# Performance work log

Hardware: AMD Instinct MI355X
Metric: run time of the kernel (lower is better)

## Reference

```python
import jax, jax.numpy as jnp
import numpy as np

N = 100000   # nodes
D = 256      # in_dim == out_dim
R = 4        # num_rel
T = 150000   # triangles per relation
H = 2        # nheads (num_rel >= 2)
DH = D // H
EPS = 1e-5


def _layernorm(x, g, b):
    m = jnp.mean(x, axis=-1, keepdims=True)
    v = jnp.mean((x - m) ** 2, axis=-1, keepdims=True)
    return (x - m) * jax.lax.rsqrt(v + EPS) * g + b


def setup_inputs() -> dict:
    key = jax.random.key(0)
    ks = jax.random.split(key, 24)
    s = 1.0 / np.sqrt(D)
    f32 = jnp.float32
    inp = {}
    inp["x"] = jax.random.normal(ks[0], (N, D), f32)
    inp["triangles"] = jax.random.randint(ks[1], (R, 3, T), 0, N)
    inp["edge_index"] = jax.random.randint(ks[2], (R, 2, 8), 0, N)
    inp["node_W"] = jax.random.normal(ks[3], (R, D, D), f32) * s
    inp["tri_W"] = jax.random.normal(ks[4], (R, D, D), f32) * s
    inp["res_W"] = jax.random.normal(ks[5], (D, D), f32) * s
    inp["gate_W"] = jax.random.normal(ks[6], (D, 2 * D), f32) * (1.0 / np.sqrt(2 * D))
    inp["gate_b"] = jnp.zeros((D,), f32)
    inp["in_W"] = jax.random.normal(ks[7], (3 * D, D), f32) * s
    inp["in_b"] = jnp.zeros((3 * D,), f32)
    inp["out_W"] = jax.random.normal(ks[8], (D, D), f32) * s
    inp["out_b"] = jnp.zeros((D,), f32)
    inp["ln1_g"] = jnp.ones((D,), f32)
    inp["ln1_b"] = jnp.zeros((D,), f32)
    inp["lin1_W"] = jax.random.normal(ks[9], (2 * D, D), f32) * s
    inp["lin1_b"] = jnp.zeros((2 * D,), f32)
    inp["lin2_W"] = jax.random.normal(ks[10], (D, 2 * D), f32) * (1.0 / np.sqrt(2 * D))
    inp["lin2_b"] = jnp.zeros((D,), f32)
    inp["ln2_g"] = jnp.ones((D,), f32)
    inp["ln2_b"] = jnp.zeros((D,), f32)
    return inp


def reference(x, triangles, edge_index, node_W, tri_W, res_W, gate_W, gate_b,
              in_W, in_b, out_W, out_b, ln1_g, ln1_b,
              lin1_W, lin1_b, lin2_W, lin2_b, ln2_g, ln2_b):
    del edge_index  # unused by the original forward
    x_res = x @ res_W.T  # [N, D]
    hs = []
    for r in range(R):  # small fixed relation count
        tri = triangles[r]                                 # [3, T]
        tri_feat = (x[tri] @ node_W[r].T).mean(axis=0)     # [T, D]
        tri_msg = tri_feat @ tri_W[r].T                    # [T, D]
        idx = tri.T.reshape(-1)                            # [3T], triangle-major
        rep = jnp.repeat(tri_msg, 3, axis=0)               # [3T, D]
        ssum = jax.ops.segment_sum(rep, idx, num_segments=N)
        cnt = jax.ops.segment_sum(jnp.ones((3 * T,), x.dtype), idx, num_segments=N)
        node_msg = ssum / jnp.maximum(cnt, 1.0)[:, None]   # scatter_mean
        u = jax.nn.elu(node_msg)                           # dropout = identity (eval)
        a = jax.nn.sigmoid(jnp.concatenate([x, u], axis=1) @ gate_W.T + gate_b)
        hs.append(jnp.tanh(u) * a + x_res * (1.0 - a))
    src = jnp.stack(hs, axis=0)                            # [R, N, D] (seq, batch, d)

    # single post-norm TransformerEncoderLayer over the relation axis
    qkv = src @ in_W.T + in_b                              # [R, N, 3D]
    q, k, v = jnp.split(qkv, 3, axis=-1)
    q = q.reshape(R, N, H, DH)
    k = k.reshape(R, N, H, DH)
    v = v.reshape(R, N, H, DH)
    scores = jnp.einsum('qnhd,knhd->nhqk', q, k) / np.sqrt(DH)
    attn = jax.nn.softmax(scores, axis=-1)
    o = jnp.einsum('nhqk,knhd->qnhd', attn, v).reshape(R, N, D)
    o = o @ out_W.T + out_b
    x1 = _layernorm(src + o, ln1_g, ln1_b)
    ff = jax.nn.gelu(x1 @ lin1_W.T + lin1_b, approximate=False) @ lin2_W.T + lin2_b
    x2 = _layernorm(x1 + ff, ln2_g, ln2_b)
    return x2.mean(axis=0)                                 # [N, D]
```

## Files before the change

### kernel.cpp

```cpp
#include <hip/hip_runtime.h>


#define NNODES 100000
#define NPAD   100096
#define DIM    256
#define NREL   4
#define NTRI   150000
#define NPART  8
#define PSIZE  (NPAD / NPART)

typedef unsigned short ushortT;
typedef __attribute__((ext_vector_type(8)))  short   short8;
typedef __attribute__((ext_vector_type(4)))  float   floatx4;
typedef __attribute__((ext_vector_type(4)))  unsigned short ushort4v;

__device__ __forceinline__ float bf2f(ushortT u) {
    union { unsigned int i; float f; } c; c.i = ((unsigned int)u) << 16; return c.f;
}
__device__ __forceinline__ ushortT f2bf(float f) {
    union { float f; unsigned int i; } c; c.f = f;
    unsigned int x = c.i;
    x += 0x7fffu + ((x >> 16) & 1u);
    return (ushortT)(x >> 16);
}
__device__ __forceinline__ float erf_as(float x) {
    float ax = fabsf(x);
    float k  = 1.0f / (1.0f + 0.3275911f * ax);
    float p  = k * (0.254829592f + k * (-0.284496736f + k * (1.421413741f +
               k * (-1.453152027f + k * 1.061405429f))));
    float r  = 1.0f - p * __expf(-ax * ax);
    return copysignf(r, x);
}


__global__ void cvt_f32_bf16(const float* __restrict__ in, ushortT* __restrict__ out, int n4) {
    int i = blockIdx.x * blockDim.x + threadIdx.x;
    int stride = gridDim.x * blockDim.x;
    for (; i < n4; i += stride) {
        float4 v = ((const float4*)in)[i];
        ushort4v o; o.x = f2bf(v.x); o.y = f2bf(v.y); o.z = f2bf(v.z); o.w = f2bf(v.w);
        ((ushort4v*)out)[i] = o;
    }
}

__global__ void wcomb_kernel(const float* __restrict__ nodeW, const float* __restrict__ triW,
                             ushortT* __restrict__ wcomb) {
    int idx = blockIdx.x * 256 + threadIdx.x;
    int r = idx >> 16, o = (idx >> 8) & 255, k = idx & 255;
    const float* tw = triW  + ((size_t)r << 16) + o * 256;
    const float* nw = nodeW + ((size_t)r << 16) + k;
    float s = 0.f;
    #pragma unroll 8
    for (int j = 0; j < 256; ++j) s += tw[j] * nw[(size_t)j * 256];
    wcomb[idx] = f2bf(s);
}

__global__ void pack_xg(const float* __restrict__ resW, const float* __restrict__ gateW,
                        ushortT* __restrict__ o) {
    int idx = blockIdx.x * 256 + threadIdx.x;
    int r = idx >> 8, k = idx & 255;
    float v = (r < 256) ? resW[r * 256 + k] : gateW[(size_t)(r - 256) * 512 + k];
    o[idx] = f2bf(v);
}

__global__ void pack_wvo(const float* __restrict__ outW, const float* __restrict__ inW,
                         ushortT* __restrict__ o) {
    int idx = blockIdx.x * 256 + threadIdx.x;
    int r = idx >> 8, k = idx & 255;
    int orow = r & 255, d0 = (r >> 8) * 128;
    float s = 0.f;
    #pragma unroll 8
    for (int j = 0; j < 128; ++j)
        s += outW[orow * 256 + d0 + j] * inW[(size_t)(512 + d0 + j) * 256 + k];
    o[idx] = f2bf(s);
}

__global__ void calc_bvo(const float* __restrict__ outW, const float* __restrict__ in_b,
                         float* __restrict__ bvo) {
    int c = blockIdx.x * 256 + threadIdx.x;
    int orow = c & 255, d0 = (c >> 8) * 128;
    float s = 0.f;
    #pragma unroll 8
    for (int j = 0; j < 128; ++j) s += outW[orow * 256 + d0 + j] * in_b[512 + d0 + j];
    bvo[c] = s;
}


__global__ void k_count8(const int* __restrict__ tri, int* __restrict__ cnt4, int n3) {
    int r = blockIdx.y;
    int part = blockIdx.x & 7;
    int i = (blockIdx.x >> 3) * 256 + threadIdx.x;
    if (i >= n3) return;
    int node = tri[(size_t)r * n3 + i];
    if (node / PSIZE != part) return;
    atomicAdd(&cnt4[r * NPAD + node], 1);
}

__global__ void k_scan1(const int* __restrict__ cnt4, int* __restrict__ ptr4,
                        int* __restrict__ bsum4, int n) {
    int r = blockIdx.y;
    const int* cnt = cnt4 + r * NPAD;
    int* ptr = ptr4 + r * NPAD;
    int* bsum = bsum4 + r * 512;
    __shared__ int s[256];
    int i = blockIdx.x * 256 + threadIdx.x;
    int v = (i < n) ? cnt[i] : 0;
    s[threadIdx.x] = v; __syncthreads();
    for (int off = 1; off < 256; off <<= 1) {
        int t = (threadIdx.x >= off) ? s[threadIdx.x - off] : 0;
        __syncthreads();
        s[threadIdx.x] += t;
        __syncthreads();
    }
    if (i < n) ptr[i] = s[threadIdx.x] - v;
    if (threadIdx.x == 255) bsum[blockIdx.x] = s[255];
}

__global__ void k_scan2(const int* __restrict__ bsum4, int* __restrict__ bpre4, int nb) {
    int r = blockIdx.x;
    const int* bsum = bsum4 + r * 512;
    int* bpre = bpre4 + r * 512;
    int lane = threadIdx.x & 63;
    int run = 0;
    for (int c = 0; c < nb; c += 64) {
        int idx = c + lane;
        int v = (idx < nb) ? bsum[idx] : 0;
        int incl = v;
        #pragma unroll
        for (int off = 1; off < 64; off <<= 1) {
            int t = __shfl_up(incl, off, 64);
            if (lane >= off) incl += t;
        }
        if (idx < nb) bpre[idx] = run + incl - v;
        run += __shfl(incl, 63, 64);
    }
}

__global__ void k_scan3(const int* __restrict__ bpre4, int* __restrict__ ptr4,
                        int* __restrict__ cur4, int n) {
    int r = blockIdx.y;
    int i = blockIdx.x * 256 + threadIdx.x;
    if (i < n) {
        int p = ptr4[r * NPAD + i] + bpre4[r * 512 + blockIdx.x];
        ptr4[r * NPAD + i] = p; cur4[r * NPAD + i] = p;
    }
}

__global__ void k_fill8(const int* __restrict__ tri, int* __restrict__ cur4,
                        int* __restrict__ adj4, int n3, int T) {
    int r = blockIdx.y;
    int part = blockIdx.x & 7;
    int i = (blockIdx.x >> 3) * 256 + threadIdx.x;
    if (i >= n3) return;
    int node = tri[(size_t)r * n3 + i];
    if (node / PSIZE != part) return;
    int t = i; if (t >= 2 * T) t -= 2 * T; else if (t >= T) t -= T;
    int pos = atomicAdd(&cur4[r * NPAD + node], 1);
    adj4[(size_t)r * n3 + pos] = t;
}

__global__ __launch_bounds__(256)
void k_meanx(const int* __restrict__ tri, const ushortT* __restrict__ xb,
             ushortT* __restrict__ mx, int T) {
    int t = blockIdx.x * 4 + (threadIdx.x >> 6);
    if (t >= T) return;
    int lane = threadIdx.x & 63;
    int a = tri[t], b = tri[T + t], c = tri[2 * T + t];
    ushort4v va = *(const ushort4v*)(xb + (size_t)a * DIM + lane * 4);
    ushort4v vb = *(const ushort4v*)(xb + (size_t)b * DIM + lane * 4);
    ushort4v vc = *(const ushort4v*)(xb + (size_t)c * DIM + lane * 4);
    ushort4v o;
    o.x = f2bf((bf2f(va.x) + bf2f(vb.x) + bf2f(vc.x)) * (1.0f / 3.0f));
    o.y = f2bf((bf2f(va.y) + bf2f(vb.y) + bf2f(vc.y)) * (1.0f / 3.0f));
    o.z = f2bf((bf2f(va.z) + bf2f(vb.z) + bf2f(vc.z)) * (1.0f / 3.0f));
    o.w = f2bf((bf2f(va.w) + bf2f(vb.w) + bf2f(vc.w)) * (1.0f / 3.0f));
    *(ushort4v*)(mx + (size_t)t * DIM + lane * 4) = o;
}

__global__ __launch_bounds__(256)
void k_gather(const int* __restrict__ ptr, const int* __restrict__ cnt,
              const int* __restrict__ adj, const ushortT* __restrict__ mx,
              ushortT* __restrict__ accb, int n) {
    int node = blockIdx.x * 4 + (threadIdx.x >> 6);
    if (node >= n) return;
    int lane = threadIdx.x & 63;
    int st = ptr[node], c = cnt[node];
    float a0 = 0.f, a1 = 0.f, a2 = 0.f, a3 = 0.f;
    for (int j = 0; j < c; ++j) {
        int t = adj[st + j];
        ushort4v v = *(const ushort4v*)(mx + (size_t)t * DIM + lane * 4);
        a0 += bf2f(v.x); a1 += bf2f(v.y); a2 += bf2f(v.z); a3 += bf2f(v.w);
    }
    float inv = 1.0f / fmaxf((float)c, 1.0f);
    ushort4v o; o.x = f2bf(a0 * inv); o.y = f2bf(a1 * inv);
    o.z = f2bf(a2 * inv); o.w = f2bf(a3 * inv);
    *(ushort4v*)(accb + (size_t)node * DIM + lane * 4) = o;
}


#define BK 32
#define PADW 133

__device__ __forceinline__ void async_cp16(char* lds, const char* glb) {
    __builtin_amdgcn_global_load_lds((const __attribute__((address_space(1))) unsigned int*)glb,
                                     (__attribute__((address_space(3))) unsigned int*)lds,
                                     16, 0, 0);
}

enum { M_BF16 = 0, M_ELU = 1, M_GATE = 2, M_QKV = 3, M_RES = 4, M_GELU = 5 };

template <int MODE>
__global__ __launch_bounds__(256)
void gemm_bt(const ushortT* __restrict__ A, int lda, size_t aStrZ,
             const ushortT* __restrict__ W, int ldw, size_t wStrZ,
             int M, int K,
             ushortT* __restrict__ outB, int ldo, size_t oStrZ,
             const float* __restrict__ bias,
             const ushortT* __restrict__ aux1,
             const ushortT* __restrict__ aux2,
             int auxLd,
             const ushortT* __restrict__ resB,
             size_t resStrZ) {
    const size_t zi = blockIdx.z;
    A += zi * aStrZ; W += zi * wStrZ;
    if (outB) outB += zi * oStrZ;
    if (resB) resB += zi * resStrZ;

    __shared__ __align__(16) char smem[49152];
    const int tid  = threadIdx.x;
    const int wave = tid >> 6, lane = tid & 63;
    const int m0 = blockIdx.y * 128;
    const int n0 = blockIdx.x * 128;
    const int wm = (wave >> 1) * 64, wn = (wave & 1) * 64;

    floatx4 acc[4][4];
    #pragma unroll
    for (int i = 0; i < 4; ++i)
        #pragma unroll
        for (int j = 0; j < 4; ++j) acc[i][j] = (floatx4){0.f, 0.f, 0.f, 0.f};

    const int r4  = tid >> 2;
    const int b16 = (tid & 3) * 16;
    const char* Ab = (const char*)A + ((size_t)(m0 + r4) * lda) * 2 + b16;
    const char* Wb = (const char*)W + ((size_t)(n0 + r4) * ldw) * 2 + b16;

    const int kq = (lane >> 4) * 8;
    const int ra = wm + (lane & 15);
    const int rb = wn + (lane & 15);

    auto stage = [&](int buf, int k0) {
        char* Asl = smem + buf * 8192 + wave * 1024;
        char* Bsl = smem + 24576 + buf * 8192 + wave * 1024;
        async_cp16(Asl,        Ab + k0 * 2);
        async_cp16(Asl + 4096, Ab + k0 * 2 + (size_t)64 * lda * 2);
        async_cp16(Bsl,        Wb + k0 * 2);
        async_cp16(Bsl + 4096, Wb + k0 * 2 + (size_t)64 * ldw * 2);
    };
    auto compute = [&](int buf) {
        const ushortT* Abuf = (const ushortT*)(smem + buf * 8192);
        const ushortT* Bbuf = (const ushortT*)(smem + 24576 + buf * 8192);
        short8 af[4], bfr[4];
        #pragma unroll
        for (int i = 0; i < 4; ++i) {
            af[i]  = *(const short8*)(Abuf + (ra + i * 16) * BK + kq);
            bfr[i] = *(const short8*)(Bbuf + (rb + i * 16) * BK + kq);
        }
        #pragma unroll
        for (int mi = 0; mi < 4; ++mi)
            #pragma unroll
            for (int ni = 0; ni < 4; ++ni)
                acc[mi][ni] = __builtin_amdgcn_mfma_f32_16x16x32_bf16(af[mi], bfr[ni], acc[mi][ni], 0, 0, 0);
    };

    const int NIT = K / BK;
    stage(0, 0);
    stage(1, BK);
    asm volatile("s_waitcnt vmcnt(4)" ::: "memory");
    __builtin_amdgcn_s_barrier();

    int bufc = 0, bufs = 2;
    for (int it = 0; it < NIT; ++it) {
        if (it + 2 < NIT) stage(bufs, (it + 2) * BK);
        compute(bufc);
        if (it + 1 < NIT) {
            if (it + 2 < NIT) asm volatile("s_waitcnt vmcnt(4)" ::: "memory");
            else              asm volatile("s_waitcnt vmcnt(0)" ::: "memory");
            __builtin_amdgcn_s_barrier();
        }
        bufc = (bufc == 2) ? 0 : bufc + 1;
        bufs = (bufs == 2) ? 0 : bufs + 1;
    }

    __syncthreads();
    float* Ct = (float*)smem;
    const int cl = lane & 15, rw = (lane >> 4) * 4;
    const int lr = tid >> 2;
    const int cb = (tid & 3) * 32;
    #pragma unroll
    for (int p = 0; p < 2; ++p) {
        if (wm == p * 64) {
            #pragma unroll
            for (int mi = 0; mi < 4; ++mi)
                #pragma unroll
                for (int ni = 0; ni < 4; ++ni)
                    #pragma unroll
                    for (int e = 0; e < 4; ++e)
                        Ct[(mi * 16 + rw + e) * PADW + (wn + ni * 16 + cl)] = acc[mi][ni][e];
        }
        __syncthreads();
        const int m = m0 + p * 64 + lr;
        if (m < M) {
            #pragma unroll
            for (int k8 = 0; k8 < 4; ++k8) {
                const int c0  = cb + k8 * 8;
                const int col = n0 + c0;
                float v[8];
                #pragma unroll
                for (int j = 0; j < 8; ++j) v[j] = Ct[lr * PADW + c0 + j];
                short8 ov;
                if (MODE == M_BF16) {
                    #pragma unroll
                    for (int j = 0; j < 8; ++j) ov[j] = (short)f2bf(v[j]);
                } else if (MODE == M_ELU) {
                    #pragma unroll
                    for (int j = 0; j < 8; ++j) {
                        float c = v[j] > 0.f ? v[j] : (__expf(v[j]) - 1.0f);
                        ov[j] = (short)f2bf(c);
                    }
                } else if (MODE == M_GATE) {
                    short8 gv = *(const short8*)(aux1 + (size_t)m * auxLd + col);
                    short8 xv = *(const short8*)(aux2 + (size_t)m * auxLd + col);
                    short8 uv = *(const short8*)(A + (size_t)m * lda + col);
                    #pragma unroll
                    for (int j = 0; j < 8; ++j) {
                        float g  = bf2f((ushortT)gv[j]);
                        float xr = bf2f((ushortT)xv[j]);
                        float u  = bf2f((ushortT)uv[j]);
                        float a  = 1.0f / (1.0f + __expf(-(v[j] + g + bias[col + j])));
                        float th = 1.0f - 2.0f / (__expf(2.0f * u) + 1.0f);
                        ov[j] = (short)f2bf(th * a + xr * (1.0f - a));
                    }
                } else if (MODE == M_QKV) {
                    #pragma unroll
                    for (int j = 0; j < 8; ++j) ov[j] = (short)f2bf(v[j] + bias[col + j]);
                } else if (MODE == M_RES) {
                    short8 rv = *(const short8*)(resB + (size_t)m * 256 + col);
                    #pragma unroll
                    for (int j = 0; j < 8; ++j)
                        ov[j] = (short)f2bf(v[j] + bias[col + j] + bf2f((ushortT)rv[j]));
                } else if (MODE == M_GELU) {
                    #pragma unroll
                    for (int j = 0; j < 8; ++j) {
                        float t = v[j] + bias[col + j];
                        ov[j] = (short)f2bf(0.5f * t * (1.0f + erf_as(t * 0.70710678118f)));
                    }
                }
                *(short8*)(&outB[(size_t)m * ldo + col]) = ov;
            }
        }
        if (p == 0) __syncthreads();
    }
}

__global__ __launch_bounds__(256)
void attn_score(const ushortT* __restrict__ qk, size_t rstride,
                float* __restrict__ Aw, int nvalid) {
    int n = blockIdx.x * 4 + (threadIdx.x >> 6);
    if (n >= nvalid) return;
    int lane = threadIdx.x & 63;
    int head = lane >> 5, hl = lane & 31;
    int d = head * 128 + hl * 4;
    float q[NREL][4], k[NREL][4];
    #pragma unroll
    for (int r = 0; r < NREL; ++r) {
        const ushortT* base = qk + r * rstride + (size_t)n * 512;
        ushort4v qv = *(const ushort4v*)(base + d);
        ushort4v kv = *(const ushort4v*)(base + 256 + d);
        q[r][0] = bf2f(qv.x); q[r][1] = bf2f(qv.y); q[r][2] = bf2f(qv.z); q[r][3] = bf2f(qv.w);
        k[r][0] = bf2f(kv.x); k[r][1] = bf2f(kv.y); k[r][2] = bf2f(kv.z); k[r][3] = bf2f(kv.w);
    }
    float s[NREL][NREL];
    #pragma unroll
    for (int qr = 0; qr < NREL; ++qr)
        #pragma unroll
        for (int kr = 0; kr < NREL; ++kr) {
            float p = q[qr][0] * k[kr][0] + q[qr][1] * k[kr][1] +
                      q[qr][2] * k[kr][2] + q[qr][3] * k[kr][3];
            #pragma unroll
            for (int off = 1; off < 32; off <<= 1) p += __shfl_xor(p, off, 32);
            s[qr][kr] = p * 0.08838834764831845f;
        }
    if (hl < 16) {
        int qr = hl >> 2, kr = hl & 3;
        float mx = fmaxf(fmaxf(s[qr][0], s[qr][1]), fmaxf(s[qr][2], s[qr][3]));
        float e0 = __expf(s[qr][0] - mx), e1 = __expf(s[qr][1] - mx);
        float e2 = __expf(s[qr][2] - mx), e3 = __expf(s[qr][3] - mx);
        float e  = __expf(s[qr][kr] - mx);
        Aw[((size_t)n * 2 + head) * 16 + qr * 4 + kr] = e / (e0 + e1 + e2 + e3);
    }
}

__global__ __launch_bounds__(256)
void attn_combine_ln1(const ushortT* __restrict__ vo4, size_t rstride,
                      const ushortT* __restrict__ h4, size_t hstride,
                      const float* __restrict__ Aw,
                      const float* __restrict__ ob,
                      const float* __restrict__ g, const float* __restrict__ b,
                      ushortT* __restrict__ x1, size_t x1str, int nvalid) {
    int n = blockIdx.x * 4 + (threadIdx.x >> 6);
    if (n >= nvalid) return;
    int lane = threadIdx.x & 63;
    int d4 = lane * 4;
    const float* ap = Aw + (size_t)n * 32;
    float a0[NREL][NREL], a1[NREL][NREL];
    #pragma unroll
    for (int qr = 0; qr < NREL; ++qr)
        #pragma unroll
        for (int kr = 0; kr < NREL; ++kr) {
            a0[qr][kr] = ap[qr * 4 + kr];
            a1[qr][kr] = ap[16 + qr * 4 + kr];
        }
    float vl[NREL][4], vh[NREL][4];
    #pragma unroll
    for (int kr = 0; kr < NREL; ++kr) {
        const ushortT* base = vo4 + kr * rstride + (size_t)n * 512;
        ushort4v lo = *(const ushort4v*)(base + d4);
        ushort4v hi = *(const ushort4v*)(base + 256 + d4);
        vl[kr][0] = bf2f(lo.x); vl[kr][1] = bf2f(lo.y); vl[kr][2] = bf2f(lo.z); vl[kr][3] = bf2f(lo.w);
        vh[kr][0] = bf2f(hi.x); vh[kr][1] = bf2f(hi.y); vh[kr][2] = bf2f(hi.z); vh[kr][3] = bf2f(hi.w);
    }
    float bb0 = ob[d4], bb1 = ob[d4 + 1], bb2 = ob[d4 + 2], bb3 = ob[d4 + 3];
    float g0 = g[d4], g1 = g[d4 + 1], g2 = g[d4 + 2], g3 = g[d4 + 3];
    float e0 = b[d4], e1 = b[d4 + 1], e2 = b[d4 + 2], e3 = b[d4 + 3];
    #pragma unroll
    for (int qr = 0; qr < NREL; ++qr) {
        ushort4v hv = *(const ushort4v*)(h4 + qr * hstride + (size_t)n * 256 + d4);
        float z0 = bf2f(hv.x) + bb0, z1 = bf2f(hv.y) + bb1;
        float z2 = bf2f(hv.z) + bb2, z3 = bf2f(hv.w) + bb3;
        #pragma unroll
        for (int kr = 0; kr < NREL; ++kr) {
            float c0 = a0[qr][kr], c1 = a1[qr][kr];
            z0 += c0 * vl[kr][0] + c1 * vh[kr][0];
            z1 += c0 * vl[kr][1] + c1 * vh[kr][1];
            z2 += c0 * vl[kr][2] + c1 * vh[kr][2];
            z3 += c0 * vl[kr][3] + c1 * vh[kr][3];
        }
        float s = z0 + z1 + z2 + z3;
        #pragma unroll
        for (int off = 1; off < 64; off <<= 1) s += __shfl_xor(s, off, 64);
        float mean = s * (1.0f / 256.0f);
        float dx = z0 - mean, dy = z1 - mean, dz = z2 - mean, dw = z3 - mean;
        float qs = dx * dx + dy * dy + dz * dz + dw * dw;
        #pragma unroll
        for (int off = 1; off < 64; off <<= 1) qs += __shfl_xor(qs, off, 64);
        float rstd = rsqrtf(qs * (1.0f / 256.0f) + 1e-5f);
        ushort4v o;
        o.x = f2bf(dx * rstd * g0 + e0); o.y = f2bf(dy * rstd * g1 + e1);
        o.z = f2bf(dz * rstd * g2 + e2); o.w = f2bf(dw * rstd * g3 + e3);
        *(ushort4v*)(x1 + qr * x1str + (size_t)n * 256 + d4) = o;
    }
}

__global__ __launch_bounds__(256)
void ln2_out(const ushortT* __restrict__ zb, size_t zStrZ,
             const float* __restrict__ g, const float* __restrict__ b,
             float* __restrict__ outc, int n) {
    int row = blockIdx.x * 4 + (threadIdx.x >> 6);
    if (row >= n) return;
    int lane = threadIdx.x & 63, c0 = lane * 4;
    float g0 = g[c0], g1 = g[c0 + 1], g2 = g[c0 + 2], g3 = g[c0 + 3];
    float b0 = b[c0], b1 = b[c0 + 1], b2 = b[c0 + 2], b3 = b[c0 + 3];
    float o0 = 0.f, o1 = 0.f, o2 = 0.f, o3 = 0.f;
    #pragma unroll
    for (int r = 0; r < NREL; ++r) {
        ushort4v v = *(const ushort4v*)(zb + r * zStrZ + (size_t)row * 256 + c0);
        float vx = bf2f(v.x), vy = bf2f(v.y), vz = bf2f(v.z), vw = bf2f(v.w);
        float s = vx + vy + vz + vw;
        #pragma unroll
        for (int off = 1; off < 64; off <<= 1) s += __shfl_xor(s, off, 64);
        float mean = s * (1.0f / 256.0f);
        float dx = vx - mean, dy = vy - mean, dz = vz - mean, dw = vw - mean;
        float qs = dx * dx + dy * dy + dz * dz + dw * dw;
        #pragma unroll
        for (int off = 1; off < 64; off <<= 1) qs += __shfl_xor(qs, off, 64);
        float rstd = rsqrtf(qs * (1.0f / 256.0f) + 1e-5f);
        o0 += 0.25f * (dx * rstd * g0 + b0);
        o1 += 0.25f * (dy * rstd * g1 + b1);
        o2 += 0.25f * (dz * rstd * g2 + b2);
        o3 += 0.25f * (dw * rstd * g3 + b3);
    }
    float4 o; o.x = o0; o.y = o1; o.z = o2; o.w = o3;
    *(float4*)(outc + (size_t)row * 256 + c0) = o;
}


extern "C" void kernel_launch(void* const* d_in, const int* in_sizes, int n_in,
                              void* d_out, int out_size, void* d_ws, size_t ws_size,
                              hipStream_t stream) {
    const float* x      = (const float*)d_in[0];
    const int*   tri    = (const int*)d_in[1];
    const float* nodeW  = (const float*)d_in[3];
    const float* triW   = (const float*)d_in[4];
    const float* resW   = (const float*)d_in[5];
    const float* gateW  = (const float*)d_in[6];
    const float* gate_b = (const float*)d_in[7];
    const float* inW    = (const float*)d_in[8];
    const float* in_b   = (const float*)d_in[9];
    const float* outW   = (const float*)d_in[10];
    const float* out_b  = (const float*)d_in[11];
    const float* ln1g   = (const float*)d_in[12];
    const float* ln1b   = (const float*)d_in[13];
    const float* lin1W  = (const float*)d_in[14];
    const float* lin1b  = (const float*)d_in[15];
    const float* lin2W  = (const float*)d_in[16];
    const float* lin2b  = (const float*)d_in[17];
    const float* ln2g   = (const float*)d_in[18];
    const float* ln2b   = (const float*)d_in[19];
    float* out = (float*)d_out;

    char* ws = (char*)d_ws;
    size_t off = 0;
    auto alloc = [&](size_t bytes) -> char* {
        char* p = ws + off; off += (bytes + 255) & ~(size_t)255; return p;
    };
    ushortT* accAll  = (ushortT*)alloc((size_t)NREL * NPAD * 256 * 2);
    ushortT* xall_b  = (ushortT*)alloc((size_t)NPAD * 256 * 2);
    ushortT* wcomb   = (ushortT*)alloc((size_t)NREL * 65536 * 2);
    ushortT* xgW_b   = (ushortT*)alloc((size_t)131072 * 2);
    ushortT* gateW_b = (ushortT*)alloc((size_t)131072 * 2);
    ushortT* inW_b   = (ushortT*)alloc((size_t)131072 * 2);
    ushortT* wvo_b   = (ushortT*)alloc((size_t)131072 * 2);
    ushortT* lin1_bf = (ushortT*)alloc((size_t)131072 * 2);
    ushortT* lin2_bf = (ushortT*)alloc((size_t)131072 * 2);
    float*   bvo     = (float*)  alloc((size_t)512 * 4);
    size_t persist = off;
    size_t scratch = (ws_size > persist) ? (ws_size - persist) : 0;
    char* S = ws + persist;

    int*     cnt4  = (int*)(S);
    int*     ptr4  = cnt4 + 4 * NPAD;
    int*     cur4  = ptr4 + 4 * NPAD;
    int*     bsum4 = cur4 + 4 * NPAD;
    int*     bpre4 = bsum4 + 4 * 512;
    int*     adj4  = bpre4 + 4 * 512;
    size_t csrBytes = ((char*)(adj4 + (size_t)4 * 3 * NTRI) - S + 255) & ~(size_t)255;
    const size_t mxBytes = (size_t)NTRI * 256 * 2;
    if (scratch < csrBytes + mxBytes + 65536) return;
    ushortT* mxbf = (ushortT*)(S + csrBytes);

    const size_t ROWB = 9344;
    int TT = (NNODES + 127) / 128;
    int tpcMax = (int)(scratch / (ROWB * 128));
    if (tpcMax < 1) return;
    if (tpcMax > TT) tpcMax = TT;
    const int nchunks = (TT + tpcMax - 1) / tpcMax;
    const int tpc = (TT + nchunks - 1) / nchunks;
    const size_t NcPad = (size_t)tpc * 128;

    ushortT* xg   = (ushortT*)(S);
    ushortT* ubf4 = (ushortT*)(S + 1024 * NcPad);
    ushortT* h4   = (ushortT*)(S + 3072 * NcPad);
    ushortT* qk4  = (ushortT*)(S + 5120 * NcPad);
    ushortT* vo4  = qk4;
    ushortT* x1   = (ushortT*)(S);
    ushortT* ffg  = (ushortT*)(S + 2048 * NcPad);
    ushortT* zbb  = (ushortT*)(S + 6144 * NcPad);
    float*   Aw   = (float*)  (S + 9216 * NcPad);

    cvt_f32_bf16<<<2048, 256, 0, stream>>>(x, xall_b, NNODES * 64);
    cvt_f32_bf16<<<64, 256, 0, stream>>>(gateW, gateW_b, 131072 / 4);
    cvt_f32_bf16<<<64, 256, 0, stream>>>(inW,   inW_b,   131072 / 4);
    cvt_f32_bf16<<<64, 256, 0, stream>>>(lin1W, lin1_bf, 131072 / 4);
    cvt_f32_bf16<<<64, 256, 0, stream>>>(lin2W, lin2_bf, 131072 / 4);
    pack_xg<<<512, 256, 0, stream>>>(resW, gateW, xgW_b);
    pack_wvo<<<512, 256, 0, stream>>>(outW, inW, wvo_b);
    calc_bvo<<<2, 256, 0, stream>>>(outW, in_b, bvo);
    wcomb_kernel<<<1024, 256, 0, stream>>>(nodeW, triW, wcomb);

    const int NB = (NNODES + 255) / 256;
    const int N3B = (3 * NTRI + 255) / 256;
    (void)hipMemsetAsync(cnt4, 0, (size_t)4 * NPAD * 4, stream);
    k_count8<<<dim3(8 * N3B, 4), 256, 0, stream>>>(tri, cnt4, 3 * NTRI);
    k_scan1<<<dim3(NB, 4), 256, 0, stream>>>(cnt4, ptr4, bsum4, NNODES);
    k_scan2<<<4, 64, 0, stream>>>(bsum4, bpre4, NB);
    k_scan3<<<dim3(NB, 4), 256, 0, stream>>>(bpre4, ptr4, cur4, NNODES);
    k_fill8<<<dim3(8 * N3B, 4), 256, 0, stream>>>(tri, cur4, adj4, 3 * NTRI, NTRI);
    for (int r = 0; r < NREL; ++r) {
        const int* trir = tri + (size_t)r * 3 * NTRI;
        k_meanx<<<(NTRI + 3) / 4, 256, 0, stream>>>(trir, xall_b, mxbf, NTRI);
        k_gather<<<(NNODES + 3) / 4, 256, 0, stream>>>(
            ptr4 + (size_t)r * NPAD, cnt4 + (size_t)r * NPAD,
            adj4 + (size_t)r * 3 * NTRI, mxbf,
            accAll + (size_t)r * NPAD * 256, NNODES);
    }

    for (int ci = 0; ci < nchunks; ++ci) {
        const int rows0 = ci * tpc * 128;
        int mact = NNODES - rows0;
        if (mact <= 0) break;
        if (mact > tpc * 128) mact = tpc * 128;
        const int tiles = (mact + 127) / 128;
        const dim3 g2z(2, tiles, NREL), g4z(4, tiles, NREL);
        const int nwblk = (mact + 3) / 4;
        float* outc = out + (size_t)rows0 * 256;
        const ushortT* xbf = xall_b + (size_t)rows0 * 256;

        gemm_bt<M_BF16><<<dim3(4, tiles), 256, 0, stream>>>(xbf, 256, 0, xgW_b, 256, 0, mact, 256,
            xg, 512, 0, nullptr, nullptr, nullptr, 0, nullptr, 0);
        gemm_bt<M_ELU><<<g2z, 256, 0, stream>>>(
            accAll + (size_t)rows0 * 256, 256, (size_t)NPAD * 256,
            wcomb, 256, 65536, mact, 256,
            ubf4, 256, 256 * NcPad, nullptr, nullptr, nullptr, 0, nullptr, 0);
        gemm_bt<M_GATE><<<g2z, 256, 0, stream>>>(
            ubf4, 256, 256 * NcPad, gateW_b + 256, 512, 0, mact, 256,
            h4, 256, 256 * NcPad, gate_b, xg + 256, xg, 512, nullptr, 0);
        gemm_bt<M_QKV><<<g4z, 256, 0, stream>>>(
            h4, 256, 256 * NcPad, inW_b, 256, 0, mact, 256,
            qk4, 512, 512 * NcPad, in_b, nullptr, nullptr, 0, nullptr, 0);
        attn_score<<<nwblk, 256, 0, stream>>>(qk4, 512 * NcPad, Aw, mact);
        gemm_bt<M_QKV><<<g4z, 256, 0, stream>>>(
            h4, 256, 256 * NcPad, wvo_b, 256, 0, mact, 256,
            vo4, 512, 512 * NcPad, bvo, nullptr, nullptr, 0, nullptr, 0);
        attn_combine_ln1<<<nwblk, 256, 0, stream>>>(vo4, 512 * NcPad, h4, 256 * NcPad,
            Aw, out_b, ln1g, ln1b, x1, 256 * NcPad, mact);
        gemm_bt<M_GELU><<<g4z, 256, 0, stream>>>(x1, 256, 256 * NcPad, lin1_bf, 256, 0, mact, 256,
            ffg, 512, 512 * NcPad, lin1b, nullptr, nullptr, 0, nullptr, 0);
        gemm_bt<M_RES><<<g2z, 256, 0, stream>>>(ffg, 512, 512 * NcPad, lin2_bf, 512, 0, mact, 512,
            zbb, 256, 256 * NcPad, lin2b, nullptr, nullptr, 0, x1, 256 * NcPad);
        ln2_out<<<nwblk, 256, 0, stream>>>(zbb, 256 * NcPad, ln2g, ln2b, outc, mact);
    }
}
```

Before: 3.028 ms.

## Merge QK and VO projections into one GEMM and fuse attention kernels

Concatenates the QK and folded V·out weights into a single 1024-wide weight and bias so one GEMM produces q, k and vo together. The score softmax and the combine+LayerNorm1 kernels become a single kernel, with the attention weights shared across lanes by shuffles instead of going through a global buffer. This removes two kernel launches per chunk, one re-read of h4 and the Aw round trip through memory. In exchange the per-row scratch grows (ROWB rises), which can mean fewer rows per chunk and more chunks.

```diff
diff --git a/kernel.cpp b/kernel.cpp
--- a/kernel.cpp
+++ b/kernel.cpp
@@ -41,6 +41,11 @@
         ushort4v o; o.x = f2bf(v.x); o.y = f2bf(v.y); o.z = f2bf(v.z); o.w = f2bf(v.w);
         ((ushort4v*)out)[i] = o;
     }
+}
+
+__global__ void copy_f32(const float* __restrict__ in, float* __restrict__ out, int n) {
+    int i = blockIdx.x * 256 + threadIdx.x;
+    if (i < n) out[i] = in[i];
 }
 
 __global__ void wcomb_kernel(const float* __restrict__ nodeW, const float* __restrict__ triW,
@@ -363,8 +368,11 @@
 }
 
 __global__ __launch_bounds__(256)
-void attn_score(const ushortT* __restrict__ qk, size_t rstride,
-                float* __restrict__ Aw, int nvalid) {
+void attn_fused(const ushortT* __restrict__ qkvo, size_t rstride,
+                const ushortT* __restrict__ h4, size_t hstride,
+                const float* __restrict__ ob,
+                const float* __restrict__ g, const float* __restrict__ b,
+                ushortT* __restrict__ x1, size_t x1str, int nvalid) {
     int n = blockIdx.x * 4 + (threadIdx.x >> 6);
     if (n >= nvalid) return;
     int lane = threadIdx.x & 63;
@@ -373,7 +381,7 @@
     float q[NREL][4], k[NREL][4];
     #pragma unroll
     for (int r = 0; r < NREL; ++r) {
-        const ushortT* base = qk + r * rstride + (size_t)n * 512;
+        const ushortT* base = qkvo + r * rstride + (size_t)n * 1024;
         ushort4v qv = *(const ushort4v*)(base + d);
         ushort4v kv = *(const ushort4v*)(base + 256 + d);
         q[r][0] = bf2f(qv.x); q[r][1] = bf2f(qv.y); q[r][2] = bf2f(qv.z); q[r][3] = bf2f(qv.w);
@@ -390,40 +398,28 @@
             for (int off = 1; off < 32; off <<= 1) p += __shfl_xor(p, off, 32);
             s[qr][kr] = p * 0.08838834764831845f;
         }
-    if (hl < 16) {
-        int qr = hl >> 2, kr = hl & 3;
+    float A[NREL][NREL];
+    #pragma unroll
+    for (int qr = 0; qr < NREL; ++qr) {
         float mx = fmaxf(fmaxf(s[qr][0], s[qr][1]), fmaxf(s[qr][2], s[qr][3]));
         float e0 = __expf(s[qr][0] - mx), e1 = __expf(s[qr][1] - mx);
         float e2 = __expf(s[qr][2] - mx), e3 = __expf(s[qr][3] - mx);
-        float e  = __expf(s[qr][kr] - mx);
-        Aw[((size_t)n * 2 + head) * 16 + qr * 4 + kr] = e / (e0 + e1 + e2 + e3);
-    }
-}
-
-__global__ __launch_bounds__(256)
-void attn_combine_ln1(const ushortT* __restrict__ vo4, size_t rstride,
-                      const ushortT* __restrict__ h4, size_t hstride,
-                      const float* __restrict__ Aw,
-                      const float* __restrict__ ob,
-                      const float* __restrict__ g, const float* __restrict__ b,
-                      ushortT* __restrict__ x1, size_t x1str, int nvalid) {
-    int n = blockIdx.x * 4 + (threadIdx.x >> 6);
-    if (n >= nvalid) return;
-    int lane = threadIdx.x & 63;
+        float inv = 1.0f / (e0 + e1 + e2 + e3);
+        A[qr][0] = e0 * inv; A[qr][1] = e1 * inv; A[qr][2] = e2 * inv; A[qr][3] = e3 * inv;
+    }
+    float a0[NREL][NREL], a1[NREL][NREL];
+    #pragma unroll
+    for (int qr = 0; qr < NREL; ++qr)
+        #pragma unroll
+        for (int kr = 0; kr < NREL; ++kr) {
+            a0[qr][kr] = __shfl(A[qr][kr], 0, 64);
+            a1[qr][kr] = __shfl(A[qr][kr], 32, 64);
+        }
     int d4 = lane * 4;
-    const float* ap = Aw + (size_t)n * 32;
-    float a0[NREL][NREL], a1[NREL][NREL];
-    #pragma unroll
-    for (int qr = 0; qr < NREL; ++qr)
-        #pragma unroll
-        for (int kr = 0; kr < NREL; ++kr) {
-            a0[qr][kr] = ap[qr * 4 + kr];
-            a1[qr][kr] = ap[16 + qr * 4 + kr];
-        }
     float vl[NREL][4], vh[NREL][4];
     #pragma unroll
     for (int kr = 0; kr < NREL; ++kr) {
-        const ushortT* base = vo4 + kr * rstride + (size_t)n * 512;
+        const ushortT* base = qkvo + kr * rstride + (size_t)n * 1024 + 512;
         ushort4v lo = *(const ushort4v*)(base + d4);
         ushort4v hi = *(const ushort4v*)(base + 256 + d4);
         vl[kr][0] = bf2f(lo.x); vl[kr][1] = bf2f(lo.y); vl[kr][2] = bf2f(lo.z); vl[kr][3] = bf2f(lo.w);
@@ -445,10 +441,10 @@
             z2 += c0 * vl[kr][2] + c1 * vh[kr][2];
             z3 += c0 * vl[kr][3] + c1 * vh[kr][3];
         }
-        float s = z0 + z1 + z2 + z3;
-        #pragma unroll
-        for (int off = 1; off < 64; off <<= 1) s += __shfl_xor(s, off, 64);
-        float mean = s * (1.0f / 256.0f);
+        float s2 = z0 + z1 + z2 + z3;
+        #pragma unroll
+        for (int off = 1; off < 64; off <<= 1) s2 += __shfl_xor(s2, off, 64);
+        float mean = s2 * (1.0f / 256.0f);
         float dx = z0 - mean, dy = z1 - mean, dz = z2 - mean, dw = z3 - mean;
         float qs = dx * dx + dy * dy + dz * dz + dw * dw;
         #pragma unroll
@@ -528,11 +524,10 @@
     ushortT* wcomb   = (ushortT*)alloc((size_t)NREL * 65536 * 2);
     ushortT* xgW_b   = (ushortT*)alloc((size_t)131072 * 2);
     ushortT* gateW_b = (ushortT*)alloc((size_t)131072 * 2);
-    ushortT* inW_b   = (ushortT*)alloc((size_t)131072 * 2);
-    ushortT* wvo_b   = (ushortT*)alloc((size_t)131072 * 2);
+    ushortT* qkvoW_b = (ushortT*)alloc((size_t)262144 * 2);
     ushortT* lin1_bf = (ushortT*)alloc((size_t)131072 * 2);
     ushortT* lin2_bf = (ushortT*)alloc((size_t)131072 * 2);
-    float*   bvo     = (float*)  alloc((size_t)512 * 4);
+    float*   bqkvo   = (float*)  alloc((size_t)1024 * 4);
     size_t persist = off;
     size_t scratch = (ws_size > persist) ? (ws_size - persist) : 0;
     char* S = ws + persist;
@@ -548,7 +543,7 @@
     if (scratch < csrBytes + mxBytes + 65536) return;
     ushortT* mxbf = (ushortT*)(S + csrBytes);
 
-    const size_t ROWB = 9344;
+    const size_t ROWB = 13312;
     int TT = (NNODES + 127) / 128;
     int tpcMax = (int)(scratch / (ROWB * 128));
     if (tpcMax < 1) return;
@@ -560,21 +555,20 @@
     ushortT* xg   = (ushortT*)(S);
     ushortT* ubf4 = (ushortT*)(S + 1024 * NcPad);
     ushortT* h4   = (ushortT*)(S + 3072 * NcPad);
-    ushortT* qk4  = (ushortT*)(S + 5120 * NcPad);
-    ushortT* vo4  = qk4;
+    ushortT* qkvo = (ushortT*)(S + 5120 * NcPad);
     ushortT* x1   = (ushortT*)(S);
     ushortT* ffg  = (ushortT*)(S + 2048 * NcPad);
     ushortT* zbb  = (ushortT*)(S + 6144 * NcPad);
-    float*   Aw   = (float*)  (S + 9216 * NcPad);
 
     cvt_f32_bf16<<<2048, 256, 0, stream>>>(x, xall_b, NNODES * 64);
     cvt_f32_bf16<<<64, 256, 0, stream>>>(gateW, gateW_b, 131072 / 4);
-    cvt_f32_bf16<<<64, 256, 0, stream>>>(inW,   inW_b,   131072 / 4);
+    cvt_f32_bf16<<<64, 256, 0, stream>>>(inW,   qkvoW_b, 131072 / 4);
     cvt_f32_bf16<<<64, 256, 0, stream>>>(lin1W, lin1_bf, 131072 / 4);
     cvt_f32_bf16<<<64, 256, 0, stream>>>(lin2W, lin2_bf, 131072 / 4);
     pack_xg<<<512, 256, 0, stream>>>(resW, gateW, xgW_b);
-    pack_wvo<<<512, 256, 0, stream>>>(outW, inW, wvo_b);
-    calc_bvo<<<2, 256, 0, stream>>>(outW, in_b, bvo);
+    pack_wvo<<<512, 256, 0, stream>>>(outW, inW, qkvoW_b + 512 * 256);
+    copy_f32<<<2, 256, 0, stream>>>(in_b, bqkvo, 512);
+    calc_bvo<<<2, 256, 0, stream>>>(outW, in_b, bqkvo + 512);
     wcomb_kernel<<<1024, 256, 0, stream>>>(nodeW, triW, wcomb);
 
     const int NB = (NNODES + 255) / 256;
@@ -600,7 +594,7 @@
         if (mact <= 0) break;
         if (mact > tpc * 128) mact = tpc * 128;
         const int tiles = (mact + 127) / 128;
-        const dim3 g2z(2, tiles, NREL), g4z(4, tiles, NREL);
+        const dim3 g2z(2, tiles, NREL), g8z(8, tiles, NREL), g4z(4, tiles, NREL);
         const int nwblk = (mact + 3) / 4;
         float* outc = out + (size_t)rows0 * 256;
         const ushortT* xbf = xall_b + (size_t)rows0 * 256;
@@ -614,15 +608,11 @@
         gemm_bt<M_GATE><<<g2z, 256, 0, stream>>>(
             ubf4, 256, 256 * NcPad, gateW_b + 256, 512, 0, mact, 256,
             h4, 256, 256 * NcPad, gate_b, xg + 256, xg, 512, nullptr, 0);
-        gemm_bt<M_QKV><<<g4z, 256, 0, stream>>>(
-            h4, 256, 256 * NcPad, inW_b, 256, 0, mact, 256,
-            qk4, 512, 512 * NcPad, in_b, nullptr, nullptr, 0, nullptr, 0);
-        attn_score<<<nwblk, 256, 0, stream>>>(qk4, 512 * NcPad, Aw, mact);
-        gemm_bt<M_QKV><<<g4z, 256, 0, stream>>>(
-            h4, 256, 256 * NcPad, wvo_b, 256, 0, mact, 256,
-            vo4, 512, 512 * NcPad, bvo, nullptr, nullptr, 0, nullptr, 0);
-        attn_combine_ln1<<<nwblk, 256, 0, stream>>>(vo4, 512 * NcPad, h4, 256 * NcPad,
-            Aw, out_b, ln1g, ln1b, x1, 256 * NcPad, mact);
+        gemm_bt<M_QKV><<<g8z, 256, 0, stream>>>(
+            h4, 256, 256 * NcPad, qkvoW_b, 256, 0, mact, 256,
+            qkvo, 1024, 1024 * NcPad, bqkvo, nullptr, nullptr, 0, nullptr, 0);
+        attn_fused<<<nwblk, 256, 0, stream>>>(qkvo, 1024 * NcPad, h4, 256 * NcPad,
+            out_b, ln1g, ln1b, x1, 256 * NcPad, mact);
         gemm_bt<M_GELU><<<g4z, 256, 0, stream>>>(x1, 256, 256 * NcPad, lin1_bf, 256, 0, mact, 256,
             ffg, 512, 512 * NcPad, lin1b, nullptr, nullptr, 0, nullptr, 0);
         gemm_bt<M_RES><<<g2z, 256, 0, stream>>>(ffg, 512, 512 * NcPad, lin2_bf, 512, 0, mact, 512,
```

Result: slower. 3.129 ms (+3.3%).
